# Kernel tuning notes

Measured on AMD Instinct MI355X. Metric: run time of the kernel, lower is better.

The kernel has to match this reference:

```python
import jax, jax.numpy as jnp
import numpy as np

BN_EPS = 1e-5

def _bn_relu(x, gamma, beta):
    # training-mode BatchNorm1d: biased batch stats over (B, N) per channel
    mean = x.mean(axis=(0, 2), keepdims=True)
    var = x.var(axis=(0, 2), keepdims=True)
    xn = (x - mean) * jax.lax.rsqrt(var + BN_EPS)
    return jax.nn.relu(xn * gamma[None, :, None] + beta[None, :, None])


def setup_inputs() -> dict:
    key = jax.random.key(0)
    ks = jax.random.split(key, 12)
    B, n1, n2, c1, c2 = 16, 4096, 1024, 128, 256
    in_ch, mlp = c1 + c2, [256, 128]
    xyz1 = jax.random.uniform(ks[0], (B, n1, 3), dtype=jnp.float32)
    xyz2 = jax.random.uniform(ks[1], (B, n2, 3), dtype=jnp.float32)
    feat1 = jax.random.normal(ks[2], (B, c1, n1), dtype=jnp.float32)
    feat2 = jax.random.normal(ks[3], (B, c2, n2), dtype=jnp.float32)
    # Conv1d(k=1) weights as (out, in) matrices; kaiming-ish scale
    w0 = jax.random.normal(ks[4], (mlp[0], in_ch), dtype=jnp.float32) / np.sqrt(in_ch)
    b0 = jnp.zeros((mlp[0],), jnp.float32)
    g0 = jnp.ones((mlp[0],), jnp.float32)
    be0 = jnp.zeros((mlp[0],), jnp.float32)
    w1 = jax.random.normal(ks[5], (mlp[1], mlp[0]), dtype=jnp.float32) / np.sqrt(mlp[0])
    b1 = jnp.zeros((mlp[1],), jnp.float32)
    g1 = jnp.ones((mlp[1],), jnp.float32)
    be1 = jnp.zeros((mlp[1],), jnp.float32)
    return {"xyz1": xyz1, "xyz2": xyz2, "feat1": feat1, "feat2": feat2,
            "w0": w0, "b0": b0, "g0": g0, "be0": be0,
            "w1": w1, "b1": b1, "g1": g1, "be1": be1}


def reference(xyz1, xyz2, feat1, feat2, w0, b0, g0, be0, w1, b1, g1, be1):
    # three_nn_interpolate: squared pairwise dists (B, n1, n2)
    d = jnp.sum((xyz1[:, :, None, :] - xyz2[:, None, :, :]) ** 2, axis=-1)
    neg_d3, idx3 = jax.lax.top_k(-d, 3)          # 3 smallest dists
    d3 = -neg_d3                                  # (B, n1, 3)
    w = 1.0 / (d3 + 1e-8)
    w = w / jnp.sum(w, axis=-1, keepdims=True)
    # gather feat2 at knn indices: (B, c2, n1, 3)
    gathered = jnp.take_along_axis(feat2[:, :, None, :], idx3[:, None, :, :], axis=3)
    interp = jnp.sum(gathered * w[:, None, :, :], axis=-1)  # (B, c2, n1)

    x = jnp.concatenate([feat1, interp], axis=1)            # (B, c1+c2, n1)
    x = _bn_relu(jnp.einsum('oc,bcn->bon', w0, x) + b0[None, :, None], g0, be0)
    x = _bn_relu(jnp.einsum('oc,bcn->bon', w1, x) + b1[None, :, None], g1, be1)
    return x
```

## Files before the change

### kernel.cpp

```cpp
#include <hip/hip_runtime.h>
#include <hip/hip_bf16.h>

typedef unsigned short u16;
typedef __attribute__((ext_vector_type(8))) __bf16 bf16x8;
typedef __attribute__((ext_vector_type(4))) float floatx4;

#define B_   16
#define N1_  4096
#define N2_  1024
#define C1_  128
#define C2_  256
#define CIN_ 384
#define CM_  256
#define CO_  128

__device__ __forceinline__ u16 f2bf(float f) {
  unsigned u = __float_as_uint(f);
  u = (u + 0x7fffu + ((u >> 16) & 1u)) >> 16;
  return (u16)u;
}
__device__ __forceinline__ float bf2f(u16 h) {
  return __uint_as_float(((unsigned)h) << 16);
}

union U128 { uint4 u; bf16x8 v; u16 s[8]; };

__device__ __forceinline__ bf16x8 ldfrag(const u16* p) {
  U128 x; x.u = *(const uint4*)p; return x.v;
}
__device__ __forceinline__ uint4 pack8(const u16* h) {
  uint4 u;
  u.x = (unsigned)h[0] | ((unsigned)h[1] << 16);
  u.y = (unsigned)h[2] | ((unsigned)h[3] << 16);
  u.z = (unsigned)h[4] | ((unsigned)h[5] << 16);
  u.w = (unsigned)h[6] | ((unsigned)h[7] << 16);
  return u;
}


__global__ __launch_bounds__(256) void mega_kernel(
    const float* __restrict__ xyz1, const float* __restrict__ xyz2,
    float* __restrict__ pd, int* __restrict__ pi,
    const float* __restrict__ w0, const float* __restrict__ w1,
    u16* __restrict__ w0b, u16* __restrict__ w1b,
    const float* __restrict__ feat2, u16* __restrict__ feat2Tb,
    const float* __restrict__ feat1, u16* __restrict__ xcatT)
{
  __shared__ __align__(16) float smem[64*133];
  int t = threadIdx.x;
  int id = blockIdx.x;
  if (id < 512) {
    float4* sp = (float4*)smem;
    int xb = id & 15, b = (id >> 4) & 15, chunk = id >> 8;
    const float* p2 = xyz2 + ((size_t)b * N2_ + chunk * 512) * 3;
    #pragma unroll
    for (int l = t; l < 512; l += 256)
      sp[l] = make_float4(p2[l*3], p2[l*3+1], p2[l*3+2], 0.f);
    __syncthreads();
    int i = xb * 256 + t;
    const float* p1 = xyz1 + ((size_t)b * N1_ + i) * 3;
    float x = p1[0], y = p1[1], z = p1[2];
    float d0 = 1e30f, d1 = 1e30f, d2 = 1e30f;
    int i0 = 0, i1 = 0, i2 = 0;
    int jb = chunk * 512;
    #pragma unroll 4
    for (int j = 0; j < 512; ++j) {
      float4 p = sp[j];
      float dx = x - p.x, dy = y - p.y, dz = z - p.z;
      float d = dx*dx + dy*dy + dz*dz;
      if (d < d2) {
        int jj = jb + j;
        if (d < d0)      { d2=d1; i2=i1; d1=d0; i1=i0; d0=d; i0=jj; }
        else if (d < d1) { d2=d1; i2=i1; d1=d;  i1=jj; }
        else             { d2=d;  i2=jj; }
      }
    }
    int o = chunk*65536 + b*4096 + i;
    pd[o] = d0; pd[o + 131072] = d1; pd[o + 262144] = d2;
    pi[o] = i0; pi[o + 131072] = i1; pi[o + 262144] = i2;
    return;
  }
  if (id < 640) {
    int item = (id - 512) * 256 + t;
    if (item < 12288) {
      int m = item / 48, kc = item % 48;
      const float* p = w0 + m * CIN_ + kc * 8;
      u16 h8[8];
      #pragma unroll
      for (int j = 0; j < 8; ++j) h8[j] = f2bf(p[j]);
      int mt = m >> 4, col = m & 15, kt = kc >> 2, quad = kc & 3;
      *(uint4*)(w0b + ((mt*12 + kt)*512 + (quad*16 + col)*8)) = pack8(h8);
    } else if (item < 16384) {
      int i2 = item - 12288;
      int m = i2 >> 5, kc = i2 & 31;
      const float* p = w1 + m * CM_ + kc * 8;
      u16 h8[8];
      #pragma unroll
      for (int j = 0; j < 8; ++j) h8[j] = f2bf(p[j]);
      int mt = m >> 4, col = m & 15, kt = kc >> 2, quad = kc & 3;
      *(uint4*)(w1b + ((mt*8 + kt)*512 + (quad*16 + col)*8)) = pack8(h8);
    }
    return;
  }
  if (id < 896) {
    float (*sA2)[129] = (float(*)[129])smem;
    int idx = id - 640;
    int b = idx >> 4, n0 = (idx & 15) * 64;
    #pragma unroll 1
    for (int h = 0; h < 2; ++h) {
      if (h) __syncthreads();
      #pragma unroll
      for (int j = 0; j < 8; ++j) {
        int flat4 = t + j * 256;
        int cl = flat4 >> 4, nn4 = (flat4 & 15) * 4;
        float4 v = *(const float4*)(feat2 + ((size_t)b*C2_ + h*128 + cl)*N2_ + n0 + nn4);
        sA2[nn4+0][cl] = v.x; sA2[nn4+1][cl] = v.y; sA2[nn4+2][cl] = v.z; sA2[nn4+3][cl] = v.w;
      }
      __syncthreads();
      int nn = t & 63, chunk = t >> 6;
      u16* dst = feat2Tb + ((size_t)b*N2_ + n0 + nn)*C2_ + h*128 + chunk*32;
      #pragma unroll
      for (int g = 0; g < 4; ++g) {
        u16 h8[8];
        #pragma unroll
        for (int j = 0; j < 8; ++j) h8[j] = f2bf(sA2[nn][chunk*32 + g*8 + j]);
        *(uint4*)(dst + g*8) = pack8(h8);
      }
    }
    return;
  }
  {
    float (*sA1)[133] = (float(*)[133])smem;
    int idx = id - 896;
    int b = idx >> 6, n0 = (idx & 63) * 64;
    #pragma unroll
    for (int j = 0; j < 8; ++j) {
      int flat4 = t + j * 256;
      int c = flat4 >> 4, nn4 = (flat4 & 15) * 4;
      float4 v = *(const float4*)(feat1 + ((size_t)b*C1_ + c)*N1_ + n0 + nn4);
      sA1[nn4+0][c] = v.x; sA1[nn4+1][c] = v.y; sA1[nn4+2][c] = v.z; sA1[nn4+3][c] = v.w;
    }
    __syncthreads();
    int nn = t & 63, chunk = t >> 6;
    int n = n0 + nn, nt = n >> 4, col = n & 15;
    u16* tb = xcatT + ((size_t)b*256 + nt)*12*512;
    #pragma unroll
    for (int g = 0; g < 4; ++g) {
      int c0 = chunk*32 + g*8;
      u16 h8[8];
      #pragma unroll
      for (int j = 0; j < 8; ++j) h8[j] = f2bf(sA1[nn][c0 + j]);
      *(uint4*)(tb + (size_t)chunk*512 + (g*16 + col)*8) = pack8(h8);
    }
  }
}

__global__ __launch_bounds__(256) void interp_kernel(
    const u16* __restrict__ feat2Tb,
    const float* __restrict__ pd, const int* __restrict__ pi,
    u16* __restrict__ xcatT)
{
  __shared__ int   sidx[3][64];
  __shared__ float sw[3][64];
  int b = blockIdx.y;
  int t = threadIdx.x;
  int p0 = blockIdx.x * 64;
  if (t < 64) {
    int p = b*4096 + p0 + t;
    float d0 = 1e30f, d1 = 1e30f, d2 = 1e30f;
    int i0 = 0, i1 = 0, i2 = 0;
    #pragma unroll
    for (int c = 0; c < 2; ++c) {
      int o = c*65536 + p;
      #pragma unroll
      for (int k = 0; k < 3; ++k) {
        float d = pd[o + k*131072];
        int ix = pi[o + k*131072];
        bool c2 = d < d2, c1 = d < d1, c0 = d < d0;
        d2 = c1 ? d1 : (c2 ? d  : d2);
        i2 = c1 ? i1 : (c2 ? ix : i2);
        d1 = c0 ? d0 : (c1 ? d  : d1);
        i1 = c0 ? i0 : (c1 ? ix : i1);
        d0 = c0 ? d  : d0;
        i0 = c0 ? ix : i0;
      }
    }
    float w0 = 1.f/(d0+1e-8f), w1 = 1.f/(d1+1e-8f), w2 = 1.f/(d2+1e-8f);
    float inv = 1.f/(w0+w1+w2);
    sidx[0][t] = i0; sidx[1][t] = i1; sidx[2][t] = i2;
    sw[0][t] = w0*inv; sw[1][t] = w1*inv; sw[2][t] = w2*inv;
  }
  __syncthreads();
  int seg = t & 31;
  int pl  = t >> 5;
  #pragma unroll 2
  for (int pass = 0; pass < 8; ++pass) {
    int nl = pass*8 + pl;
    int n = p0 + nl;
    int i0 = sidx[0][nl], i1 = sidx[1][nl], i2 = sidx[2][nl];
    float w0 = sw[0][nl], w1 = sw[1][nl], w2 = sw[2][nl];
    const u16* fb = feat2Tb + (size_t)b*N2_*C2_ + seg*8;
    U128 a, c, d;
    a.u = *(const uint4*)(fb + (size_t)i0*C2_);
    c.u = *(const uint4*)(fb + (size_t)i1*C2_);
    d.u = *(const uint4*)(fb + (size_t)i2*C2_);
    u16 h8[8];
    #pragma unroll
    for (int j = 0; j < 8; ++j)
      h8[j] = f2bf(w0*bf2f(a.s[j]) + w1*bf2f(c.s[j]) + w2*bf2f(d.s[j]));
    int nt = n >> 4, col = n & 15;
    int kt = 4 + (seg >> 2), quad = seg & 3;
    *(uint4*)(xcatT + (((size_t)b*256 + nt)*12 + kt)*512 + (quad*16 + col)*8) = pack8(h8);
  }
}

__global__ __launch_bounds__(256) void gemm1_mfma(
    const u16* __restrict__ xcatT, const u16* __restrict__ w0b,
    const float* __restrict__ b0p, u16* __restrict__ y0T,
    float* __restrict__ p0)
{
  __shared__ float ps[4][64][2];
  int t = threadIdx.x;
  int wave = t >> 6, lane = t & 63;
  int col = lane & 15, quad = lane >> 4;
  int wm = wave >> 1, wn = wave & 1;
  int b = blockIdx.y;
  int mtb = blockIdx.z*8 + wm*4;
  int ntb = blockIdx.x*8 + wn*4;

  const u16* ap = w0b + lane*8;
  const u16* bp = xcatT + ((size_t)(b*256 + ntb)*12)*512 + lane*8;

  floatx4 acc[4][4] = {};
  bf16x8 aA[4], aB[4], aC[4], bA[4], bB[4], bC[4];

#define G1_LDA(BUF, KT) { _Pragma("unroll") for (int i = 0; i < 4; ++i) \
    BUF[i] = ldfrag(ap + (size_t)((mtb+i)*12 + (KT))*512); }
#define G1_LDB(BUF, KT) { _Pragma("unroll") for (int i = 0; i < 4; ++i) \
    BUF[i] = ldfrag(bp + (size_t)(i*12 + (KT))*512); }
#define G1_MM(A_, B_) { _Pragma("unroll") for (int mt = 0; mt < 4; ++mt) \
    _Pragma("unroll") for (int nt = 0; nt < 4; ++nt) \
      acc[mt][nt] = __builtin_amdgcn_mfma_f32_16x16x32_bf16(A_[mt], B_[nt], acc[mt][nt], 0, 0, 0); }

  G1_LDA(aA,0);  G1_LDB(bA,0);
  G1_LDA(aB,1);  G1_LDB(bB,1);
  G1_LDA(aC,2);  G1_LDB(bC,2);
  G1_MM(aA,bA);  G1_LDA(aA,3);  G1_LDB(bA,3);
  G1_MM(aB,bB);  G1_LDA(aB,4);  G1_LDB(bB,4);
  G1_MM(aC,bC);  G1_LDA(aC,5);  G1_LDB(bC,5);
  G1_MM(aA,bA);  G1_LDA(aA,6);  G1_LDB(bA,6);
  G1_MM(aB,bB);  G1_LDA(aB,7);  G1_LDB(bB,7);
  G1_MM(aC,bC);  G1_LDA(aC,8);  G1_LDB(bC,8);
  G1_MM(aA,bA);  G1_LDA(aA,9);  G1_LDB(bA,9);
  G1_MM(aB,bB);  G1_LDA(aB,10); G1_LDB(bB,10);
  G1_MM(aC,bC);  G1_LDA(aC,11); G1_LDB(bC,11);
  G1_MM(aA,bA);
  G1_MM(aB,bB);
  G1_MM(aC,bC);

  int m0 = blockIdx.z*128 + wm*64;
  #pragma unroll
  for (int mt = 0; mt < 4; ++mt) {
    float4 bias4 = *(const float4*)(b0p + m0 + mt*16 + quad*4);
    float bia[4] = {bias4.x, bias4.y, bias4.z, bias4.w};
    int kt_out = (m0 >> 5) + (mt >> 1);
    int quad_out = ((mt & 1) << 1) | (quad >> 1);
    int j0 = (quad & 1) * 4;
    float s[4] = {}, q[4] = {};
    #pragma unroll
    for (int nt = 0; nt < 4; ++nt) {
      int nt_g = ntb + nt;
      u16 h[4];
      #pragma unroll
      for (int r = 0; r < 4; ++r) {
        float v = acc[mt][nt][r] + bia[r];
        u16 hh = f2bf(v);
        float vr = bf2f(hh);
        h[r] = hh; s[r] += vr; q[r] += vr*vr;
      }
      *(ushort4*)(y0T + (((size_t)b*256 + nt_g)*8 + kt_out)*512 + (quad_out*16 + col)*8 + j0)
          = make_ushort4(h[0], h[1], h[2], h[3]);
    }
    #pragma unroll
    for (int r = 0; r < 4; ++r) {
      float ss = s[r], qq = q[r];
      #pragma unroll
      for (int msk = 1; msk < 16; msk <<= 1) { ss += __shfl_xor(ss, msk); qq += __shfl_xor(qq, msk); }
      if (col == 0) {
        ps[wave][mt*16 + quad*4 + r][0] = ss;
        ps[wave][mt*16 + quad*4 + r][1] = qq;
      }
    }
  }
  __syncthreads();
  {
    int c = t >> 1, k = t & 1;
    int wbase = (c >> 6) * 2, ch = c & 63;
    float v = ps[wbase][ch][k] + ps[wbase+1][ch][k];
    size_t l = (size_t)blockIdx.z*512 + blockIdx.y*32 + blockIdx.x;
    p0[l*256 + t] = v;
  }
}

__global__ __launch_bounds__(256) void stats_kernel(
    const float* __restrict__ p, const float* __restrict__ g,
    const float* __restrict__ be, float* __restrict__ scale,
    float* __restrict__ shift, int half_split, int nl)
{
  int c = blockIdx.x, t = threadIdx.x;
  size_t base = half_split ? ((size_t)(c >> 7) * 512 * 256 + (size_t)(c & 127) * 2)
                           : ((size_t)c * 2);
  float s = 0.f, q = 0.f;
  for (int i = 0; i < nl; ++i) {
    float2 v = *(const float2*)(p + base + (size_t)(t + i*256) * 256);
    s += v.x; q += v.y;
  }
  #pragma unroll
  for (int m = 1; m < 64; m <<= 1) { s += __shfl_xor(s, m); q += __shfl_xor(q, m); }
  __shared__ float2 red[4];
  if ((t & 63) == 0) red[t >> 6] = make_float2(s, q);
  __syncthreads();
  if (t == 0) {
    float ss = red[0].x + red[1].x + red[2].x + red[3].x;
    float qq = red[0].y + red[1].y + red[2].y + red[3].y;
    float mu  = ss * (1.f/65536.f);
    float var = qq * (1.f/65536.f) - mu*mu;
    float a = g[c] * rsqrtf(var + 1e-5f);
    scale[c] = a; shift[c] = be[c] - mu*a;
  }
}

__global__ __launch_bounds__(256) void gemm2_mfma(
    const u16* __restrict__ y0T, const u16* __restrict__ w1b,
    const float* __restrict__ b1p,
    const float* __restrict__ scale0, const float* __restrict__ shift0,
    float* __restrict__ out, float* __restrict__ p1)
{
  __shared__ float a0s[CM_], bb0s[CM_];
  __shared__ float ps[4][64][2];
  int t = threadIdx.x;
  a0s[t] = scale0[t]; bb0s[t] = shift0[t];
  __syncthreads();
  int wave = t >> 6, lane = t & 63;
  int col = lane & 15, quad = lane >> 4;
  int wm = wave >> 1, wn = wave & 1;
  int b = blockIdx.y;
  int mtb = wm*4;
  int ntb = blockIdx.x*8 + wn*4;

  const u16* ap = w1b + lane*8;
  const u16* bp = y0T + ((size_t)(b*256 + ntb)*8)*512 + lane*8;

  floatx4 acc[4][4] = {};
  bf16x8 aA[4], aB[4], aC[4];
  U128 rA[4], rB[4], rC[4];

#define G2_LDA(BUF, KT) { _Pragma("unroll") for (int i = 0; i < 4; ++i) \
    BUF[i] = ldfrag(ap + (size_t)((mtb+i)*8 + (KT))*512); }
#define G2_LDB(BUF, KT) { _Pragma("unroll") for (int i = 0; i < 4; ++i) \
    BUF[i].u = *(const uint4*)(bp + (size_t)(i*8 + (KT))*512); }
#define G2_BNMM(A_, R_, KT) { \
    int c0 = (KT)*32 + quad*8; \
    float av[8], bv[8]; \
    *(float4*)&av[0] = *(const float4*)&a0s[c0];  *(float4*)&av[4] = *(const float4*)&a0s[c0+4]; \
    *(float4*)&bv[0] = *(const float4*)&bb0s[c0]; *(float4*)&bv[4] = *(const float4*)&bb0s[c0+4]; \
    bf16x8 bfv[4]; \
    _Pragma("unroll") for (int j = 0; j < 4; ++j) { \
      u16 h8[8]; \
      _Pragma("unroll") for (int e = 0; e < 8; ++e) \
        h8[e] = f2bf(fmaxf(fmaf(bf2f(R_[j].s[e]), av[e], bv[e]), 0.f)); \
      U128 x_; x_.u = pack8(h8); bfv[j] = x_.v; } \
    _Pragma("unroll") for (int mt = 0; mt < 4; ++mt) \
    _Pragma("unroll") for (int nt = 0; nt < 4; ++nt) \
      acc[mt][nt] = __builtin_amdgcn_mfma_f32_16x16x32_bf16(A_[mt], bfv[nt], acc[mt][nt], 0, 0, 0); }

  G2_LDA(aA,0);  G2_LDB(rA,0);
  G2_LDA(aB,1);  G2_LDB(rB,1);
  G2_LDA(aC,2);  G2_LDB(rC,2);
  G2_BNMM(aA,rA,0);  G2_LDA(aA,3);  G2_LDB(rA,3);
  G2_BNMM(aB,rB,1);  G2_LDA(aB,4);  G2_LDB(rB,4);
  G2_BNMM(aC,rC,2);  G2_LDA(aC,5);  G2_LDB(rC,5);
  G2_BNMM(aA,rA,3);  G2_LDA(aA,6);  G2_LDB(rA,6);
  G2_BNMM(aB,rB,4);  G2_LDA(aB,7);  G2_LDB(rB,7);
  G2_BNMM(aC,rC,5);
  G2_BNMM(aA,rA,6);
  G2_BNMM(aB,rB,7);

  int m0 = wm*64;
  int n0 = blockIdx.x*128 + wn*64;
  #pragma unroll
  for (int mt = 0; mt < 4; ++mt) {
    float4 bias4 = *(const float4*)(b1p + m0 + mt*16 + quad*4);
    float bia[4] = {bias4.x, bias4.y, bias4.z, bias4.w};
    float s[4] = {}, q[4] = {};
    #pragma unroll
    for (int nt = 0; nt < 4; ++nt) {
      int n = n0 + nt*16 + col;
      #pragma unroll
      for (int r = 0; r < 4; ++r) {
        float v = acc[mt][nt][r] + bia[r];
        out[((size_t)b*CO_ + m0 + mt*16 + quad*4 + r)*N1_ + n] = v;
        s[r] += v; q[r] += v*v;
      }
    }
    #pragma unroll
    for (int r = 0; r < 4; ++r) {
      float ss = s[r], qq = q[r];
      #pragma unroll
      for (int msk = 1; msk < 16; msk <<= 1) { ss += __shfl_xor(ss, msk); qq += __shfl_xor(qq, msk); }
      if (col == 0) {
        ps[wave][mt*16 + quad*4 + r][0] = ss;
        ps[wave][mt*16 + quad*4 + r][1] = qq;
      }
    }
  }
  __syncthreads();
  {
    int c = t >> 1, k = t & 1;
    int wbase = (c >> 6) * 2, ch = c & 63;
    float v = ps[wbase][ch][k] + ps[wbase+1][ch][k];
    size_t l = (size_t)blockIdx.y*32 + blockIdx.x;
    p1[l*256 + t] = v;
  }
}

__global__ __launch_bounds__(256) void bnrelu_kernel(
    float* __restrict__ out, const float* __restrict__ scale1, const float* __restrict__ shift1)
{
  int idx = blockIdx.x * 256 + threadIdx.x;
  int c = (idx >> 10) & (CO_ - 1);
  float a = scale1[c];
  float bb = shift1[c];
  float4 v = ((const float4*)out)[idx];
  v.x = fmaxf(fmaf(v.x, a, bb), 0.f);
  v.y = fmaxf(fmaf(v.y, a, bb), 0.f);
  v.z = fmaxf(fmaf(v.z, a, bb), 0.f);
  v.w = fmaxf(fmaf(v.w, a, bb), 0.f);
  ((float4*)out)[idx] = v;
}

extern "C" void kernel_launch(void* const* d_in, const int* in_sizes, int n_in,
                              void* d_out, int out_size, void* d_ws, size_t ws_size,
                              hipStream_t stream)
{
  const float* xyz1  = (const float*)d_in[0];
  const float* xyz2  = (const float*)d_in[1];
  const float* feat1 = (const float*)d_in[2];
  const float* feat2 = (const float*)d_in[3];
  const float* w0    = (const float*)d_in[4];
  const float* b0    = (const float*)d_in[5];
  const float* g0    = (const float*)d_in[6];
  const float* be0   = (const float*)d_in[7];
  const float* w1    = (const float*)d_in[8];
  const float* b1    = (const float*)d_in[9];
  const float* g1    = (const float*)d_in[10];
  const float* be1   = (const float*)d_in[11];
  float* out = (float*)d_out;
  char* ws = (char*)d_ws;

  u16*   xcatT   = (u16*)ws;
  float* p1      = (float*)ws;
  u16*   y0T     = (u16*)(ws + 50331648);
  u16*   feat2Tb = (u16*)(ws + 50331648);
  float* knn_pd  = (float*)(ws + 58720256);
  int*   knn_pi  = (int*)(ws + 65011712);
  u16*   w0b     = (u16*)(ws + 83886080);
  u16*   w1b     = (u16*)(ws + 84082688);
  float* p0      = (float*)(ws + 85721088);
  float* scale0  = (float*)(ws + 87293952);
  float* shift0  = scale0 + 256;
  float* scale1  = scale0 + 512;
  float* shift1  = scale0 + 640;

  mega_kernel  <<<1920,           256, 0, stream>>>(xyz1, xyz2, knn_pd, knn_pi, w0, w1,
                                                    w0b, w1b, feat2, feat2Tb, feat1, xcatT);
  interp_kernel<<<dim3(64,16),    256, 0, stream>>>(feat2Tb, knn_pd, knn_pi, xcatT);
  gemm1_mfma   <<<dim3(32,16,2),  256, 0, stream>>>(xcatT, w0b, b0, y0T, p0);
  stats_kernel <<<256,            256, 0, stream>>>(p0, g0, be0, scale0, shift0, 1, 2);
  gemm2_mfma   <<<dim3(32,16),    256, 0, stream>>>(y0T, w1b, b1, scale0, shift0, out, p1);
  stats_kernel <<<128,            256, 0, stream>>>(p1, g1, be1, scale1, shift1, 0, 2);
  bnrelu_kernel<<<8192,           256, 0, stream>>>(out, scale1, shift1);
}
```

Baseline: 253.2 us.

## Replace brute-force 3-NN with uniform-grid spatial binning and ring search

Adds a bin_kernel that sorts xyz2 points into an 8x8x8 uniform grid per batch with a prefix-sum of cell counts. The kNN part of mega_kernel now searches cells in expanding Chebyshev rings around the query cell and stops once the third-best distance is below the ring bound, instead of scanning all 1024 points in two chunks. It also computes the interpolation weights directly, which removes the chunk-merge step from interp_kernel. The cost is an extra launch, data-dependent loops with warp divergence, and a grid sized for coordinates in [0,1).

```diff
diff --git a/kernel.cpp b/kernel.cpp
--- a/kernel.cpp
+++ b/kernel.cpp
@@ -38,9 +38,56 @@
 }
 
 
+__global__ __launch_bounds__(256) void bin_kernel(
+    const float* __restrict__ xyz2, float4* __restrict__ binned,
+    int* __restrict__ cellstart)
+{
+  __shared__ float4 pts[1024];
+  __shared__ int cid[1024];
+  __shared__ int cnt[512];
+  __shared__ int pairincl[256];
+  __shared__ int starts[513];
+  __shared__ int cur[512];
+  int b = blockIdx.x, t = threadIdx.x;
+  cnt[t] = 0; cnt[t + 256] = 0;
+  __syncthreads();
+  for (int k = t; k < 1024; k += 256) {
+    const float* p = xyz2 + ((size_t)b * N2_ + k) * 3;
+    float x = p[0], y = p[1], z = p[2];
+    int cx = min(7, max(0, (int)(x * 8.f)));
+    int cy = min(7, max(0, (int)(y * 8.f)));
+    int cz = min(7, max(0, (int)(z * 8.f)));
+    int c = (cz * 8 + cy) * 8 + cx;
+    pts[k] = make_float4(x, y, z, __int_as_float(k));
+    cid[k] = c;
+    atomicAdd(&cnt[c], 1);
+  }
+  __syncthreads();
+  pairincl[t] = cnt[2*t] + cnt[2*t+1];
+  __syncthreads();
+  for (int off = 1; off < 256; off <<= 1) {
+    int v = (t >= off) ? pairincl[t - off] : 0;
+    __syncthreads();
+    pairincl[t] += v;
+    __syncthreads();
+  }
+  int excl = (t == 0) ? 0 : pairincl[t-1];
+  starts[2*t]   = excl;
+  starts[2*t+1] = excl + cnt[2*t];
+  if (t == 0) starts[512] = 1024;
+  cur[2*t] = starts[2*t]; cur[2*t+1] = starts[2*t+1];
+  __syncthreads();
+  for (int k = t; k < 1024; k += 256) {
+    int pos = atomicAdd(&cur[cid[k]], 1);
+    binned[(size_t)b * N2_ + pos] = pts[k];
+  }
+  for (int l = t; l < 513; l += 256) cellstart[b * 513 + l] = starts[l];
+}
+
 __global__ __launch_bounds__(256) void mega_kernel(
-    const float* __restrict__ xyz1, const float* __restrict__ xyz2,
-    float* __restrict__ pd, int* __restrict__ pi,
+    const float* __restrict__ xyz1,
+    const float4* __restrict__ binned, const int* __restrict__ cellstart,
+    int* __restrict__ idx_out, float* __restrict__ w_out,
     const float* __restrict__ w0, const float* __restrict__ w1,
     u16* __restrict__ w0b, u16* __restrict__ w1b,
     const float* __restrict__ feat2, u16* __restrict__ feat2Tb,
@@ -49,39 +96,68 @@
   __shared__ __align__(16) float smem[64*133];
   int t = threadIdx.x;
   int id = blockIdx.x;
-  if (id < 512) {
+  if (id < 256) {
     float4* sp = (float4*)smem;
-    int xb = id & 15, b = (id >> 4) & 15, chunk = id >> 8;
-    const float* p2 = xyz2 + ((size_t)b * N2_ + chunk * 512) * 3;
-    #pragma unroll
-    for (int l = t; l < 512; l += 256)
-      sp[l] = make_float4(p2[l*3], p2[l*3+1], p2[l*3+2], 0.f);
+    int* cs = (int*)&smem[4096];
+    int b = id >> 4, xb = id & 15;
+    for (int l = t; l < 1024; l += 256) sp[l] = binned[(size_t)b * N2_ + l];
+    for (int l = t; l < 513; l += 256) cs[l] = cellstart[b * 513 + l];
     __syncthreads();
     int i = xb * 256 + t;
     const float* p1 = xyz1 + ((size_t)b * N1_ + i) * 3;
     float x = p1[0], y = p1[1], z = p1[2];
+    int cx = min(7, max(0, (int)(x * 8.f)));
+    int cy = min(7, max(0, (int)(y * 8.f)));
+    int cz = min(7, max(0, (int)(z * 8.f)));
     float d0 = 1e30f, d1 = 1e30f, d2 = 1e30f;
     int i0 = 0, i1 = 0, i2 = 0;
-    int jb = chunk * 512;
-    #pragma unroll 4
-    for (int j = 0; j < 512; ++j) {
-      float4 p = sp[j];
-      float dx = x - p.x, dy = y - p.y, dz = z - p.z;
-      float d = dx*dx + dy*dy + dz*dz;
-      if (d < d2) {
-        int jj = jb + j;
-        if (d < d0)      { d2=d1; i2=i1; d1=d0; i1=i0; d0=d; i0=jj; }
-        else if (d < d1) { d2=d1; i2=i1; d1=d;  i1=jj; }
-        else             { d2=d;  i2=jj; }
-      }
-    }
-    int o = chunk*65536 + b*4096 + i;
-    pd[o] = d0; pd[o + 131072] = d1; pd[o + 262144] = d2;
-    pi[o] = i0; pi[o + 131072] = i1; pi[o + 262144] = i2;
+    #pragma unroll 1
+    for (int r = 0; r <= 7; ++r) {
+      if (r > 0) {
+        float bnd = (float)(r - 1) * 0.125f;
+        if (d2 < bnd * bnd) break;
+      }
+      int zlo = max(cz - r, 0), zhi = min(cz + r, 7);
+      int ylo = max(cy - r, 0), yhi = min(cy + r, 7);
+      int xlo = max(cx - r, 0), xhi = min(cx + r, 7);
+      for (int ccz = zlo; ccz <= zhi; ++ccz) {
+        int az = ccz > cz ? ccz - cz : cz - ccz;
+        for (int ccy = ylo; ccy <= yhi; ++ccy) {
+          int ay = ccy > cy ? ccy - cy : cy - ccy;
+          int aym = max(az, ay);
+          for (int ccx = xlo; ccx <= xhi; ++ccx) {
+            int ax = ccx > cx ? ccx - cx : cx - ccx;
+            if (max(aym, ax) != r) continue;
+            int c = (ccz * 8 + ccy) * 8 + ccx;
+            int s = cs[c], e = cs[c + 1];
+            for (int k = s; k < e; ++k) {
+              float4 p = sp[k];
+              float ddx = x - p.x, ddy = y - p.y, ddz = z - p.z;
+              float d = ddx*ddx + ddy*ddy + ddz*ddz;
+              int jj = __float_as_int(p.w);
+              if (d < d2 || (d == d2 && jj < i2)) {
+                if (d < d0 || (d == d0 && jj < i0))      { d2=d1; i2=i1; d1=d0; i1=i0; d0=d; i0=jj; }
+                else if (d < d1 || (d == d1 && jj < i1)) { d2=d1; i2=i1; d1=d;  i1=jj; }
+                else                                     { d2=d;  i2=jj; }
+              }
+            }
+          }
+        }
+      }
+    }
+    float w0_ = 1.f/(d0+1e-8f), w1_ = 1.f/(d1+1e-8f), w2_ = 1.f/(d2+1e-8f);
+    float inv = 1.f/(w0_+w1_+w2_);
+    int pidx = b * N1_ + i;
+    idx_out[pidx]          = i0;
+    idx_out[pidx +  65536] = i1;
+    idx_out[pidx + 131072] = i2;
+    w_out[pidx]            = w0_*inv;
+    w_out[pidx +  65536]   = w1_*inv;
+    w_out[pidx + 131072]   = w2_*inv;
     return;
   }
-  if (id < 640) {
-    int item = (id - 512) * 256 + t;
+  if (id < 384) {
+    int item = (id - 256) * 256 + t;
     if (item < 12288) {
       int m = item / 48, kc = item % 48;
       const float* p = w0 + m * CIN_ + kc * 8;
@@ -102,9 +178,9 @@
     }
     return;
   }
-  if (id < 896) {
+  if (id < 640) {
     float (*sA2)[129] = (float(*)[129])smem;
-    int idx = id - 640;
+    int idx = id - 384;
     int b = idx >> 4, n0 = (idx & 15) * 64;
     #pragma unroll 1
     for (int h = 0; h < 2; ++h) {
@@ -131,7 +207,7 @@
   }
   {
     float (*sA1)[133] = (float(*)[133])smem;
-    int idx = id - 896;
+    int idx = id - 640;
     int b = idx >> 6, n0 = (idx & 63) * 64;
     #pragma unroll
     for (int j = 0; j < 8; ++j) {
@@ -157,48 +233,20 @@
 
 __global__ __launch_bounds__(256) void interp_kernel(
     const u16* __restrict__ feat2Tb,
-    const float* __restrict__ pd, const int* __restrict__ pi,
+    const int* __restrict__ idx_in, const float* __restrict__ w_in,
     u16* __restrict__ xcatT)
 {
-  __shared__ int   sidx[3][64];
-  __shared__ float sw[3][64];
   int b = blockIdx.y;
   int t = threadIdx.x;
   int p0 = blockIdx.x * 64;
-  if (t < 64) {
-    int p = b*4096 + p0 + t;
-    float d0 = 1e30f, d1 = 1e30f, d2 = 1e30f;
-    int i0 = 0, i1 = 0, i2 = 0;
-    #pragma unroll
-    for (int c = 0; c < 2; ++c) {
-      int o = c*65536 + p;
-      #pragma unroll
-      for (int k = 0; k < 3; ++k) {
-        float d = pd[o + k*131072];
-        int ix = pi[o + k*131072];
-        bool c2 = d < d2, c1 = d < d1, c0 = d < d0;
-        d2 = c1 ? d1 : (c2 ? d  : d2);
-        i2 = c1 ? i1 : (c2 ? ix : i2);
-        d1 = c0 ? d0 : (c1 ? d  : d1);
-        i1 = c0 ? i0 : (c1 ? ix : i1);
-        d0 = c0 ? d  : d0;
-        i0 = c0 ? ix : i0;
-      }
-    }
-    float w0 = 1.f/(d0+1e-8f), w1 = 1.f/(d1+1e-8f), w2 = 1.f/(d2+1e-8f);
-    float inv = 1.f/(w0+w1+w2);
-    sidx[0][t] = i0; sidx[1][t] = i1; sidx[2][t] = i2;
-    sw[0][t] = w0*inv; sw[1][t] = w1*inv; sw[2][t] = w2*inv;
-  }
-  __syncthreads();
   int seg = t & 31;
   int pl  = t >> 5;
   #pragma unroll 2
   for (int pass = 0; pass < 8; ++pass) {
-    int nl = pass*8 + pl;
-    int n = p0 + nl;
-    int i0 = sidx[0][nl], i1 = sidx[1][nl], i2 = sidx[2][nl];
-    float w0 = sw[0][nl], w1 = sw[1][nl], w2 = sw[2][nl];
+    int n = p0 + pass*8 + pl;
+    int base = b*N1_ + n;
+    int i0 = idx_in[base], i1 = idx_in[base + 65536], i2 = idx_in[base + 131072];
+    float w0 = w_in[base], w1 = w_in[base + 65536], w2 = w_in[base + 131072];
     const u16* fb = feat2Tb + (size_t)b*N2_*C2_ + seg*8;
     U128 a, c, d;
     a.u = *(const uint4*)(fb + (size_t)i0*C2_);
@@ -462,19 +510,22 @@
   float* p1      = (float*)ws;
   u16*   y0T     = (u16*)(ws + 50331648);
   u16*   feat2Tb = (u16*)(ws + 50331648);
-  float* knn_pd  = (float*)(ws + 58720256);
-  int*   knn_pi  = (int*)(ws + 65011712);
   u16*   w0b     = (u16*)(ws + 83886080);
   u16*   w1b     = (u16*)(ws + 84082688);
+  int*   idx_buf = (int*)(ws + 84148224);
+  float* w_buf   = (float*)(ws + 84934656);
   float* p0      = (float*)(ws + 85721088);
+  float4* binned = (float4*)(ws + 86769664);
+  int*   cellst  = (int*)(ws + 87031808);
   float* scale0  = (float*)(ws + 87293952);
   float* shift0  = scale0 + 256;
   float* scale1  = scale0 + 512;
   float* shift1  = scale0 + 640;
 
-  mega_kernel  <<<1920,           256, 0, stream>>>(xyz1, xyz2, knn_pd, knn_pi, w0, w1,
-                                                    w0b, w1b, feat2, feat2Tb, feat1, xcatT);
-  interp_kernel<<<dim3(64,16),    256, 0, stream>>>(feat2Tb, knn_pd, knn_pi, xcatT);
+  bin_kernel   <<<16,             256, 0, stream>>>(xyz2, binned, cellst);
+  mega_kernel  <<<1664,           256, 0, stream>>>(xyz1, binned, cellst, idx_buf, w_buf,
+                                                    w0, w1, w0b, w1b, feat2, feat2Tb, feat1, xcatT);
+  interp_kernel<<<dim3(64,16),    256, 0, stream>>>(feat2Tb, idx_buf, w_buf, xcatT);
   gemm1_mfma   <<<dim3(32,16,2),  256, 0, stream>>>(xcatT, w0b, b0, y0T, p0);
   stats_kernel <<<256,            256, 0, stream>>>(p0, g0, be0, scale0, shift0, 1, 2);
   gemm2_mfma   <<<dim3(32,16),    256, 0, stream>>>(y0T, w1b, b1, scale0, shift0, out, p1);
```

Measured after the change: 303.8 us. 20.0% more time.
